# Performance work log

Measured on AMD Instinct MI355X. Metric: run time of the kernel, lower is better.

## Reference

```python
import jax, jax.numpy as jnp
import numpy as np

ALIGN_SCALE = 3.0
UNIF_SCALE = 1.0
EPS = 1e-12  # torch F.normalize eps


def _normalize(x):
    n = jnp.linalg.norm(x, axis=-1, keepdims=True)
    return x / jnp.maximum(n, EPS)


def _unif_loss(a, b):
    # log(mean(exp(-2 * ||a_i - b_j||^2))) over all N*M pairs, fused via GEMM identity
    sq_a = jnp.sum(a * a, axis=1)  # [N]
    sq_b = jnp.sum(b * b, axis=1)  # [M]
    # squared distances: ||a||^2 + ||b||^2 - 2 a.b, clipped at 0 for numerics
    d2 = jnp.maximum(sq_a[:, None] + sq_b[None, :] - 2.0 * (a @ b.T), 0.0)  # [N, M]
    return jnp.log(jnp.mean(jnp.exp(-2.0 * d2)))


def setup_inputs() -> dict:
    key = jax.random.key(0)
    k1, k2 = jax.random.split(key)
    N, D = 8192, 512
    return {
        "image_embed": jax.random.normal(k1, (N, D), dtype=jnp.float32),
        "text_embed": jax.random.normal(k2, (N, D), dtype=jnp.float32),
    }


def reference(image_embed, text_embed):
    img = _normalize(image_embed)
    txt = _normalize(text_embed)
    # alignment: mean squared L2 between paired embeddings
    diff = img - txt
    align_loss = jnp.mean(jnp.sum(diff * diff, axis=1))
    # single device: gathered-all tensors equal the local tensors
    text_unif = _unif_loss(txt, txt)
    image_unif = _unif_loss(img, img)
    unif_loss = (text_unif + image_unif) / 2.0
    return ALIGN_SCALE * align_loss + UNIF_SCALE * unif_loss
```

## Files before the change

kernel.cpp:

```cpp
#include <hip/hip_runtime.h>
#include <hip/hip_bf16.h>


#define NROWS 8192
#define DBYTES 256
#define NBLK  1056
#define SCALE4 0x7B7B7B7B

typedef __attribute__((ext_vector_type(8)))  int   int8v;
typedef __attribute__((ext_vector_type(4)))  int   int4v;
typedef __attribute__((ext_vector_type(16))) float float16v;

__device__ inline void load_lds16(const void* g, void* l) {
    __builtin_amdgcn_global_load_lds(
        (const __attribute__((address_space(1))) void*)g,
        (__attribute__((address_space(3))) void*)l, 16, 0, 0);
}

__device__ inline int swz(int r) { return (r ^ (r >> 3)) & 7; }

__device__ inline unsigned fp4_code(float x) {
    const float a = fabsf(x);
    unsigned c = (a < 0.25f) ? 0u : (a < 0.75f) ? 1u : (a < 1.25f) ? 2u :
                 (a < 1.75f) ? 3u : (a < 2.5f)  ? 4u : (a < 3.5f)  ? 5u :
                 (a < 5.0f)  ? 6u : 7u;
    return c | ((__float_as_uint(x) >> 28) & 8u);
}

__global__ __launch_bounds__(256) void normalize_kernel(
    const float* __restrict__ img, const float* __restrict__ txt,
    int* __restrict__ nimg, int* __restrict__ ntxt,
    float* __restrict__ alignp,
    float* __restrict__ S)
{
    if (blockIdx.x == 0 && threadIdx.x < 64) S[threadIdx.x] = 0.0f;

    const int lane = threadIdx.x & 63;
    const int wave = threadIdx.x >> 6;
    const int row  = blockIdx.x * 4 + wave;

    const float4* pi = (const float4*)(img + (size_t)row * 512);
    const float4* pt = (const float4*)(txt + (size_t)row * 512);
    const float4 i0 = pi[2 * lane], i1 = pi[2 * lane + 1];
    const float4 t0 = pt[2 * lane], t1 = pt[2 * lane + 1];

    float ssi = i0.x*i0.x + i0.y*i0.y + i0.z*i0.z + i0.w*i0.w
              + i1.x*i1.x + i1.y*i1.y + i1.z*i1.z + i1.w*i1.w;
    float sst = t0.x*t0.x + t0.y*t0.y + t0.z*t0.z + t0.w*t0.w
              + t1.x*t1.x + t1.y*t1.y + t1.z*t1.z + t1.w*t1.w;
    float dot = i0.x*t0.x + i0.y*t0.y + i0.z*t0.z + i0.w*t0.w
              + i1.x*t1.x + i1.y*t1.y + i1.z*t1.z + i1.w*t1.w;

    #pragma unroll
    for (int off = 1; off < 64; off <<= 1) {
        ssi += __shfl_xor(ssi, off);
        sst += __shfl_xor(sst, off);
        dot += __shfl_xor(dot, off);
    }
    const float inv_i = 1.0f / fmaxf(sqrtf(ssi), 1e-12f);
    const float inv_t = 1.0f / fmaxf(sqrtf(sst), 1e-12f);
    const float si = 16.0f * inv_i;
    const float st = 16.0f * inv_t;

    unsigned wi = 0, wt = 0;
    wi |= fp4_code(i0.x * si)       | (fp4_code(i0.y * si) << 4)
       |  (fp4_code(i0.z * si) << 8)| (fp4_code(i0.w * si) << 12)
       |  (fp4_code(i1.x * si) <<16)| (fp4_code(i1.y * si) << 20)
       |  (fp4_code(i1.z * si) <<24)| (fp4_code(i1.w * si) << 28);
    wt |= fp4_code(t0.x * st)       | (fp4_code(t0.y * st) << 4)
       |  (fp4_code(t0.z * st) << 8)| (fp4_code(t0.w * st) << 12)
       |  (fp4_code(t1.x * st) <<16)| (fp4_code(t1.y * st) << 20)
       |  (fp4_code(t1.z * st) <<24)| (fp4_code(t1.w * st) << 28);

    nimg[row * 64 + lane] = (int)wi;
    ntxt[row * 64 + lane] = (int)wt;

    __shared__ float r4[4];
    if (lane == 0) r4[wave] = dot * inv_i * inv_t;
    __syncthreads();
    if (threadIdx.x == 0)
        alignp[blockIdx.x] = r4[0] + r4[1] + r4[2] + r4[3];
}

__global__ __launch_bounds__(256, 2) void gram_kernel(
    const unsigned char* __restrict__ A0,
    const unsigned char* __restrict__ A1,
    float* __restrict__ S)
{
    const int b = blockIdx.x;
    int I = (int)((65.0f - sqrtf(4225.0f - 4.0f * (float)b)) * 0.5f);
    while ((I + 1) * (64 - I) <= b) ++I;
    while (I * (65 - I) > b) --I;
    const int j = 2 * I + (b - I * (65 - I));

    const unsigned char* __restrict__ A = blockIdx.y ? A1 : A0;
    const int tid  = threadIdx.x;
    const int lane = tid & 63;
    const int wave = tid >> 6;
    const int wm = wave & 1, wn = wave >> 1;
    const int lr = lane & 31;
    const int h  = lane >> 5;

    const unsigned char* gA = A + (size_t)I * 256 * DBYTES;
    const unsigned char* gB = A + (size_t)j * 128 * DBYTES;

    __shared__ __align__(16) unsigned char ldsA[256 * 128];
    __shared__ __align__(16) unsigned char ldsB[128 * 128];

    float16v acc[4][2];
    #pragma unroll
    for (int a = 0; a < 4; ++a)
        #pragma unroll
        for (int c = 0; c < 2; ++c)
            #pragma unroll
            for (int r = 0; r < 16; ++r) acc[a][c][r] = 0.0f;

    for (int k0 = 0; k0 < DBYTES; k0 += 128) {
        #pragma unroll
        for (int rnd = 0; rnd < 8; ++rnd) {
            const int slot = rnd * 4096 + tid * 16;
            const int r    = slot >> 7;
            const int cp   = (slot >> 4) & 7;
            const int cl   = cp ^ swz(r);
            load_lds16(gA + (size_t)r * DBYTES + k0 + cl * 16, &ldsA[slot]);
        }
        #pragma unroll
        for (int rnd = 0; rnd < 4; ++rnd) {
            const int slot = rnd * 4096 + tid * 16;
            const int r    = slot >> 7;
            const int cp   = (slot >> 4) & 7;
            const int cl   = cp ^ swz(r);
            load_lds16(gB + (size_t)r * DBYTES + k0 + cl * 16, &ldsB[slot]);
        }
        __syncthreads();

        #pragma unroll
        for (int kk = 0; kk < 4; ++kk) {
            const int c0 = kk * 2 + h;
            int8v av[4], bv[2];
            #pragma unroll
            for (int mt = 0; mt < 4; ++mt) {
                const int r = wm * 128 + mt * 32 + lr;
                *((int4v*)&av[mt]) =
                    *(const int4v*)&ldsA[r * 128 + (c0 ^ swz(r)) * 16];
                *((int4v*)&av[mt] + 1) = (int4v){0, 0, 0, 0};
            }
            #pragma unroll
            for (int nt = 0; nt < 2; ++nt) {
                const int r = wn * 64 + nt * 32 + lr;
                *((int4v*)&bv[nt]) =
                    *(const int4v*)&ldsB[r * 128 + (c0 ^ swz(r)) * 16];
                *((int4v*)&bv[nt] + 1) = (int4v){0, 0, 0, 0};
            }
            #pragma unroll
            for (int mt = 0; mt < 4; ++mt)
                #pragma unroll
                for (int nt = 0; nt < 2; ++nt)
                    acc[mt][nt] = __builtin_amdgcn_mfma_scale_f32_32x32x64_f8f6f4(
                        av[mt], bv[nt], acc[mt][nt],
                        4, 4,
                        0, SCALE4,
                        0, SCALE4);
        }
        __syncthreads();
    }

    const int r128 = 2 * I + wm;
    const float wv = (j > r128) ? 2.0f : ((j == r128) ? 1.0f : 0.0f);
    float s = 0.0f;
    #pragma unroll
    for (int mt = 0; mt < 4; ++mt)
        #pragma unroll
        for (int nt = 0; nt < 2; ++nt)
            #pragma unroll
            for (int r2 = 0; r2 < 16; ++r2) {
                const float g = acc[mt][nt][r2];
                s += __expf(4.0f * fminf(g, 1.0f) - 4.0f);
            }
    s *= wv;
    #pragma unroll
    for (int off = 32; off; off >>= 1) s += __shfl_down(s, off);
    __shared__ float ps[4];
    if (lane == 0) ps[wave] = s;
    __syncthreads();
    if (tid == 0) {
        const float tot = ps[0] + ps[1] + ps[2] + ps[3];
        atomicAdd(&S[blockIdx.y * 32 + (blockIdx.x & 31)], tot);
    }
}

__global__ __launch_bounds__(256) void finalize_kernel(
    const float* __restrict__ S,
    const float* __restrict__ alignp,
    float* __restrict__ out)
{
    const int tid = threadIdx.x;
    float a = 0.0f;
    #pragma unroll
    for (int k = 0; k < 8; ++k) a += alignp[tid + 256 * k];
    #pragma unroll
    for (int off = 32; off; off >>= 1) a += __shfl_down(a, off);
    __shared__ float r4[4];
    if ((tid & 63) == 0) r4[tid >> 6] = a;
    __syncthreads();
    if (tid == 0) {
        const double A = (double)r4[0] + r4[1] + r4[2] + r4[3];
        double si = 0.0, st = 0.0;
        for (int k = 0; k < 32; ++k) { si += S[k]; st += S[32 + k]; }
        const double align = 2.0 - 2.0 * A / (double)NROWS;
        const double n2 = (double)NROWS * (double)NROWS;
        const double unif = 0.5 * (log(si / n2) + log(st / n2));
        out[0] = (float)(3.0 * align + unif);
    }
}

extern "C" void kernel_launch(void* const* d_in, const int* in_sizes, int n_in,
                              void* d_out, int out_size, void* d_ws, size_t ws_size,
                              hipStream_t stream) {
    const float* img = (const float*)d_in[0];
    const float* txt = (const float*)d_in[1];
    char* ws = (char*)d_ws;
    int* nimg = (int*)ws;
    int* ntxt = (int*)(ws + (size_t)NROWS * DBYTES);
    float* S      = (float*)(ws + 2 * (size_t)NROWS * DBYTES);
    float* alignp = S + 64;

    normalize_kernel<<<NROWS / 4, 256, 0, stream>>>(img, txt, nimg, ntxt, alignp, S);
    dim3 grid(NBLK, 2);
    gram_kernel<<<grid, 256, 0, stream>>>((const unsigned char*)nimg,
                                          (const unsigned char*)ntxt, S);
    finalize_kernel<<<1, 256, 0, stream>>>(S, alignp, (float*)d_out);
}
```

Measured before the change: 111.2 us.

## Use 512-thread gram blocks with both K stages prefetched into LDS

Doubles the gram kernel block to 8 waves, each computing a 64x64 sub-tile, which halves per-wave accumulator registers. Both K halves are loaded into separate LDS buffers up front, with a vmcnt wait on only the first half so the second half's loads overlap the first half's MFMAs. This removes a per-iteration barrier pair but doubles LDS use to 96KB per block, which may limit residency to fewer blocks per CU.

```diff
diff --git a/kernel.cpp b/kernel.cpp
--- a/kernel.cpp
+++ b/kernel.cpp
@@ -82,7 +82,7 @@
         alignp[blockIdx.x] = r4[0] + r4[1] + r4[2] + r4[3];
 }
 
-__global__ __launch_bounds__(256, 2) void gram_kernel(
+__global__ __launch_bounds__(512, 2) void gram_kernel(
     const unsigned char* __restrict__ A0,
     const unsigned char* __restrict__ A1,
     float* __restrict__ S)
@@ -97,63 +97,74 @@
     const int tid  = threadIdx.x;
     const int lane = tid & 63;
     const int wave = tid >> 6;
-    const int wm = wave & 1, wn = wave >> 1;
+    const int wm = wave & 3;
+    const int wn = wave >> 2;
     const int lr = lane & 31;
     const int h  = lane >> 5;
 
     const unsigned char* gA = A + (size_t)I * 256 * DBYTES;
     const unsigned char* gB = A + (size_t)j * 128 * DBYTES;
 
-    __shared__ __align__(16) unsigned char ldsA[256 * 128];
-    __shared__ __align__(16) unsigned char ldsB[128 * 128];
-
-    float16v acc[4][2];
-    #pragma unroll
-    for (int a = 0; a < 4; ++a)
+    __shared__ __align__(16) unsigned char ldsA[2][256 * 128];
+    __shared__ __align__(16) unsigned char ldsB[2][128 * 128];
+
+    float16v acc[2][2];
+    #pragma unroll
+    for (int a = 0; a < 2; ++a)
         #pragma unroll
         for (int c = 0; c < 2; ++c)
             #pragma unroll
             for (int r = 0; r < 16; ++r) acc[a][c][r] = 0.0f;
 
-    for (int k0 = 0; k0 < DBYTES; k0 += 128) {
-        #pragma unroll
-        for (int rnd = 0; rnd < 8; ++rnd) {
-            const int slot = rnd * 4096 + tid * 16;
+    #pragma unroll
+    for (int s = 0; s < 2; ++s) {
+        const int k0 = s * 128;
+        #pragma unroll
+        for (int rnd = 0; rnd < 4; ++rnd) {
+            const int slot = rnd * 8192 + tid * 16;
             const int r    = slot >> 7;
             const int cp   = (slot >> 4) & 7;
             const int cl   = cp ^ swz(r);
-            load_lds16(gA + (size_t)r * DBYTES + k0 + cl * 16, &ldsA[slot]);
-        }
-        #pragma unroll
-        for (int rnd = 0; rnd < 4; ++rnd) {
-            const int slot = rnd * 4096 + tid * 16;
+            load_lds16(gA + (size_t)r * DBYTES + k0 + cl * 16, &ldsA[s][slot]);
+        }
+        #pragma unroll
+        for (int rnd = 0; rnd < 2; ++rnd) {
+            const int slot = rnd * 8192 + tid * 16;
             const int r    = slot >> 7;
             const int cp   = (slot >> 4) & 7;
             const int cl   = cp ^ swz(r);
-            load_lds16(gB + (size_t)r * DBYTES + k0 + cl * 16, &ldsB[slot]);
-        }
-        __syncthreads();
-
+            load_lds16(gB + (size_t)r * DBYTES + k0 + cl * 16, &ldsB[s][slot]);
+        }
+        __builtin_amdgcn_sched_barrier(0);
+    }
+
+    asm volatile("s_waitcnt vmcnt(6)" ::: "memory");
+    __builtin_amdgcn_sched_barrier(0);
+    __builtin_amdgcn_s_barrier();
+    __builtin_amdgcn_sched_barrier(0);
+
+    #pragma unroll
+    for (int s = 0; s < 2; ++s) {
         #pragma unroll
         for (int kk = 0; kk < 4; ++kk) {
             const int c0 = kk * 2 + h;
-            int8v av[4], bv[2];
-            #pragma unroll
-            for (int mt = 0; mt < 4; ++mt) {
-                const int r = wm * 128 + mt * 32 + lr;
+            int8v av[2], bv[2];
+            #pragma unroll
+            for (int mt = 0; mt < 2; ++mt) {
+                const int r = wm * 64 + mt * 32 + lr;
                 *((int4v*)&av[mt]) =
-                    *(const int4v*)&ldsA[r * 128 + (c0 ^ swz(r)) * 16];
+                    *(const int4v*)&ldsA[s][r * 128 + (c0 ^ swz(r)) * 16];
                 *((int4v*)&av[mt] + 1) = (int4v){0, 0, 0, 0};
             }
             #pragma unroll
             for (int nt = 0; nt < 2; ++nt) {
                 const int r = wn * 64 + nt * 32 + lr;
                 *((int4v*)&bv[nt]) =
-                    *(const int4v*)&ldsB[r * 128 + (c0 ^ swz(r)) * 16];
+                    *(const int4v*)&ldsB[s][r * 128 + (c0 ^ swz(r)) * 16];
                 *((int4v*)&bv[nt] + 1) = (int4v){0, 0, 0, 0};
             }
             #pragma unroll
-            for (int mt = 0; mt < 4; ++mt)
+            for (int mt = 0; mt < 2; ++mt)
                 #pragma unroll
                 for (int nt = 0; nt < 2; ++nt)
                     acc[mt][nt] = __builtin_amdgcn_mfma_scale_f32_32x32x64_f8f6f4(
@@ -162,14 +173,18 @@
                         0, SCALE4,
                         0, SCALE4);
         }
-        __syncthreads();
-    }
-
-    const int r128 = 2 * I + wm;
+        if (s == 0) {
+            asm volatile("s_waitcnt vmcnt(0)" ::: "memory");
+            __builtin_amdgcn_s_barrier();
+            __builtin_amdgcn_sched_barrier(0);
+        }
+    }
+
+    const int r128 = 2 * I + (wm >> 1);
     const float wv = (j > r128) ? 2.0f : ((j == r128) ? 1.0f : 0.0f);
     float s = 0.0f;
     #pragma unroll
-    for (int mt = 0; mt < 4; ++mt)
+    for (int mt = 0; mt < 2; ++mt)
         #pragma unroll
         for (int nt = 0; nt < 2; ++nt)
             #pragma unroll
@@ -180,11 +195,12 @@
     s *= wv;
     #pragma unroll
     for (int off = 32; off; off >>= 1) s += __shfl_down(s, off);
-    __shared__ float ps[4];
+    __shared__ float ps[8];
     if (lane == 0) ps[wave] = s;
     __syncthreads();
     if (tid == 0) {
-        const float tot = ps[0] + ps[1] + ps[2] + ps[3];
+        const float tot = ps[0] + ps[1] + ps[2] + ps[3]
+                        + ps[4] + ps[5] + ps[6] + ps[7];
         atomicAdd(&S[blockIdx.y * 32 + (blockIdx.x & 31)], tot);
     }
 }
@@ -227,7 +243,7 @@
 
     normalize_kernel<<<NROWS / 4, 256, 0, stream>>>(img, txt, nimg, ntxt, alignp, S);
     dim3 grid(NBLK, 2);
-    gram_kernel<<<grid, 256, 0, stream>>>((const unsigned char*)nimg,
+    gram_kernel<<<grid, 512, 0, stream>>>((const unsigned char*)nimg,
                                           (const unsigned char*)ntxt, S);
     finalize_kernel<<<1, 256, 0, stream>>>(S, alignp, (float*)d_out);
 }
```

New measurement: 120.9 us. 1.09x slower.

## Replace LDS-staged 256x128 gram tiles with direct-to-register 128x128 triangular tiles

Applied to the files above, without the earlier changes.

The gram kernel drops the LDS staging (global_load_lds plus swizzle and barriers). Each wave now loads its FP4 operand fragments straight from global memory into registers, double-buffered across the 8 k-steps. Tiles shrink from 256x128 to 128x128 over the upper triangle, which means 2080 blocks and an exact diagonal weight. This removes LDS traffic and synchronisation and improves load balance, but it loses data reuse across waves, so each A/B row is read by two waves directly from L2/global memory.

```diff
diff --git a/kernel.cpp b/kernel.cpp
--- a/kernel.cpp
+++ b/kernel.cpp
@@ -4,20 +4,12 @@
 
 #define NROWS 8192
 #define DBYTES 256
-#define NBLK  1056
+#define NTRI  2080
 #define SCALE4 0x7B7B7B7B
 
 typedef __attribute__((ext_vector_type(8)))  int   int8v;
 typedef __attribute__((ext_vector_type(4)))  int   int4v;
 typedef __attribute__((ext_vector_type(16))) float float16v;
-
-__device__ inline void load_lds16(const void* g, void* l) {
-    __builtin_amdgcn_global_load_lds(
-        (const __attribute__((address_space(1))) void*)g,
-        (__attribute__((address_space(3))) void*)l, 16, 0, 0);
-}
-
-__device__ inline int swz(int r) { return (r ^ (r >> 3)) & 7; }
 
 __device__ inline unsigned fp4_code(float x) {
     const float a = fabsf(x);
@@ -87,13 +79,6 @@
     const unsigned char* __restrict__ A1,
     float* __restrict__ S)
 {
-    const int b = blockIdx.x;
-    int I = (int)((65.0f - sqrtf(4225.0f - 4.0f * (float)b)) * 0.5f);
-    while ((I + 1) * (64 - I) <= b) ++I;
-    while (I * (65 - I) > b) --I;
-    const int j = 2 * I + (b - I * (65 - I));
-
-    const unsigned char* __restrict__ A = blockIdx.y ? A1 : A0;
     const int tid  = threadIdx.x;
     const int lane = tid & 63;
     const int wave = tid >> 6;
@@ -101,92 +86,82 @@
     const int lr = lane & 31;
     const int h  = lane >> 5;
 
-    const unsigned char* gA = A + (size_t)I * 256 * DBYTES;
-    const unsigned char* gB = A + (size_t)j * 128 * DBYTES;
-
-    __shared__ __align__(16) unsigned char ldsA[256 * 128];
-    __shared__ __align__(16) unsigned char ldsB[128 * 128];
-
-    float16v acc[4][2];
-    #pragma unroll
-    for (int a = 0; a < 4; ++a)
+    const int tt = blockIdx.x;
+    int i = (int)((129.0f - sqrtf(16641.0f - 8.0f * (float)tt)) * 0.5f);
+    while (64 * (i + 1) - ((i + 1) * i) / 2 <= tt) ++i;
+    while (64 * i - (i * (i - 1)) / 2 > tt) --i;
+    const int j = i + (tt - (64 * i - (i * (i - 1)) / 2));
+
+    const unsigned char* __restrict__ M = blockIdx.y ? A1 : A0;
+
+    const int4v* qa0 = (const int4v*)(M +
+        ((size_t)(i * 128 + wm * 64 + lr)) * DBYTES + h * 16);
+    const int4v* qa1 = (const int4v*)((const unsigned char*)qa0 + 32 * DBYTES);
+    const int4v* qb0 = (const int4v*)(M +
+        ((size_t)(j * 128 + wn * 64 + lr)) * DBYTES + h * 16);
+    const int4v* qb1 = (const int4v*)((const unsigned char*)qb0 + 32 * DBYTES);
+
+    float16v acc[2][2];
+    #pragma unroll
+    for (int a = 0; a < 2; ++a)
         #pragma unroll
         for (int c = 0; c < 2; ++c)
             #pragma unroll
             for (int r = 0; r < 16; ++r) acc[a][c][r] = 0.0f;
 
-    for (int k0 = 0; k0 < DBYTES; k0 += 128) {
-        #pragma unroll
-        for (int rnd = 0; rnd < 8; ++rnd) {
-            const int slot = rnd * 4096 + tid * 16;
-            const int r    = slot >> 7;
-            const int cp   = (slot >> 4) & 7;
-            const int cl   = cp ^ swz(r);
-            load_lds16(gA + (size_t)r * DBYTES + k0 + cl * 16, &ldsA[slot]);
+    int8v a0w[2], a1w[2], b0w[2], b1w[2];
+    #pragma unroll
+    for (int q = 0; q < 2; ++q) {
+        a0w[q] = (int8v){0,0,0,0,0,0,0,0};
+        a1w[q] = (int8v){0,0,0,0,0,0,0,0};
+        b0w[q] = (int8v){0,0,0,0,0,0,0,0};
+        b1w[q] = (int8v){0,0,0,0,0,0,0,0};
+    }
+    *(int4v*)&a0w[0] = qa0[0];
+    *(int4v*)&a1w[0] = qa1[0];
+    *(int4v*)&b0w[0] = qb0[0];
+    *(int4v*)&b1w[0] = qb1[0];
+
+    #pragma unroll
+    for (int kk = 0; kk < 8; ++kk) {
+        const int w = kk & 1;
+        if (kk < 7) {
+            *(int4v*)&a0w[w ^ 1] = qa0[2 * (kk + 1)];
+            *(int4v*)&a1w[w ^ 1] = qa1[2 * (kk + 1)];
+            *(int4v*)&b0w[w ^ 1] = qb0[2 * (kk + 1)];
+            *(int4v*)&b1w[w ^ 1] = qb1[2 * (kk + 1)];
         }
-        #pragma unroll
-        for (int rnd = 0; rnd < 4; ++rnd) {
-            const int slot = rnd * 4096 + tid * 16;
-            const int r    = slot >> 7;
-            const int cp   = (slot >> 4) & 7;
-            const int cl   = cp ^ swz(r);
-            load_lds16(gB + (size_t)r * DBYTES + k0 + cl * 16, &ldsB[slot]);
-        }
-        __syncthreads();
-
-        #pragma unroll
-        for (int kk = 0; kk < 4; ++kk) {
-            const int c0 = kk * 2 + h;
-            int8v av[4], bv[2];
-            #pragma unroll
-            for (int mt = 0; mt < 4; ++mt) {
-                const int r = wm * 128 + mt * 32 + lr;
-                *((int4v*)&av[mt]) =
-                    *(const int4v*)&ldsA[r * 128 + (c0 ^ swz(r)) * 16];
-                *((int4v*)&av[mt] + 1) = (int4v){0, 0, 0, 0};
-            }
-            #pragma unroll
-            for (int nt = 0; nt < 2; ++nt) {
-                const int r = wn * 64 + nt * 32 + lr;
-                *((int4v*)&bv[nt]) =
-                    *(const int4v*)&ldsB[r * 128 + (c0 ^ swz(r)) * 16];
-                *((int4v*)&bv[nt] + 1) = (int4v){0, 0, 0, 0};
-            }
-            #pragma unroll
-            for (int mt = 0; mt < 4; ++mt)
-                #pragma unroll
-                for (int nt = 0; nt < 2; ++nt)
-                    acc[mt][nt] = __builtin_amdgcn_mfma_scale_f32_32x32x64_f8f6f4(
-                        av[mt], bv[nt], acc[mt][nt],
-                        4, 4,
-                        0, SCALE4,
-                        0, SCALE4);
-        }
-        __syncthreads();
-    }
-
-    const int r128 = 2 * I + wm;
-    const float wv = (j > r128) ? 2.0f : ((j == r128) ? 1.0f : 0.0f);
-    float s = 0.0f;
-    #pragma unroll
-    for (int mt = 0; mt < 4; ++mt)
+        acc[0][0] = __builtin_amdgcn_mfma_scale_f32_32x32x64_f8f6f4(
+            a0w[w], b0w[w], acc[0][0], 4, 4, 0, SCALE4, 0, SCALE4);
+        acc[0][1] = __builtin_amdgcn_mfma_scale_f32_32x32x64_f8f6f4(
+            a0w[w], b1w[w], acc[0][1], 4, 4, 0, SCALE4, 0, SCALE4);
+        acc[1][0] = __builtin_amdgcn_mfma_scale_f32_32x32x64_f8f6f4(
+            a1w[w], b0w[w], acc[1][0], 4, 4, 0, SCALE4, 0, SCALE4);
+        acc[1][1] = __builtin_amdgcn_mfma_scale_f32_32x32x64_f8f6f4(
+            a1w[w], b1w[w], acc[1][1], 4, 4, 0, SCALE4, 0, SCALE4);
+    }
+
+    const float wgt = (j > i) ? 2.0f : 1.0f;
+    float f = 0.0f;
+    #pragma unroll
+    for (int mt = 0; mt < 2; ++mt)
         #pragma unroll
         for (int nt = 0; nt < 2; ++nt)
             #pragma unroll
             for (int r2 = 0; r2 < 16; ++r2) {
                 const float g = acc[mt][nt][r2];
-                s += __expf(4.0f * fminf(g, 1.0f) - 4.0f);
+                f += __expf(4.0f * fminf(g, 1.0f) - 4.0f);
             }
-    s *= wv;
-    #pragma unroll
-    for (int off = 32; off; off >>= 1) s += __shfl_down(s, off);
+    f *= wgt;
+    #pragma unroll
+    for (int off = 32; off; off >>= 1) f += __shfl_down(f, off);
+
     __shared__ float ps[4];
-    if (lane == 0) ps[wave] = s;
+    if (lane == 0) ps[wave] = f;
     __syncthreads();
-    if (tid == 0) {
-        const float tot = ps[0] + ps[1] + ps[2] + ps[3];
-        atomicAdd(&S[blockIdx.y * 32 + (blockIdx.x & 31)], tot);
-    }
+    if (tid == 0)
+        atomicAdd(&S[blockIdx.y * 32 + (blockIdx.x & 31)],
+                  ps[0] + ps[1] + ps[2] + ps[3]);
 }
 
 __global__ __launch_bounds__(256) void finalize_kernel(
@@ -226,8 +201,7 @@
     float* alignp = S + 64;
 
     normalize_kernel<<<NROWS / 4, 256, 0, stream>>>(img, txt, nimg, ntxt, alignp, S);
-    dim3 grid(NBLK, 2);
-    gram_kernel<<<grid, 256, 0, stream>>>((const unsigned char*)nimg,
-                                          (const unsigned char*)ntxt, S);
+    gram_kernel<<<dim3(NTRI, 2), 256, 0, stream>>>(
+        (const unsigned char*)nimg, (const unsigned char*)ntxt, S);
     finalize_kernel<<<1, 256, 0, stream>>>(S, alignp, (float*)d_out);
 }
```

New measurement: 141.7 us. 1.27x slower.
